# Performance work log

Measured on AMD Instinct MI355X. Metric: run time of the kernel, lower is better.

Reference implementation:

```python
import jax, jax.numpy as jnp
import numpy as np

DIM = 2048
N_HEADS = 16
HEAD_DIM = 128
KV_HEADS = 1
ROPE_BASE = 10000.0


def _rope_tables(T, dim, dtype):
    inv_freq = 1.0 / (ROPE_BASE ** (jnp.arange(0, dim, 2, dtype=jnp.float32) / dim))
    t = jnp.arange(T, dtype=jnp.float32)
    freqs = jnp.einsum('i,j->ij', t, inv_freq)          # [T, dim/2]
    emb = jnp.concatenate([freqs, freqs], axis=-1)      # [T, dim]
    cos = jnp.cos(emb)[None, None, :, :].astype(dtype)  # [1,1,T,dim]
    sin = jnp.sin(emb)[None, None, :, :].astype(dtype)
    return cos, sin


def _rotate_half(x):
    x1, x2 = jnp.split(x, 2, axis=-1)
    return jnp.concatenate([-x2, x1], axis=-1)


def setup_inputs() -> dict:
    key = jax.random.key(0)
    k1, k2, k3, k4, k5 = jax.random.split(key, 5)
    B, T = 2, 2048
    x = jax.random.normal(k1, (B, T, DIM), dtype=jnp.float32)
    # additive causal mask: 0 on/below diagonal, -1e9 above
    causal = jnp.triu(jnp.full((T, T), -1e9, dtype=jnp.float32), k=1)
    attn_mask = causal[None, None, :, :]
    s = 1.0 / np.sqrt(DIM)
    wq = jax.random.normal(k2, (DIM, N_HEADS * HEAD_DIM), dtype=jnp.float32) * s
    wk = jax.random.normal(k3, (DIM, KV_HEADS * HEAD_DIM), dtype=jnp.float32) * s
    wv = jax.random.normal(k4, (DIM, KV_HEADS * HEAD_DIM), dtype=jnp.float32) * s
    wo = jax.random.normal(k5, (N_HEADS * HEAD_DIM, DIM), dtype=jnp.float32) * s
    return {"x": x, "attn_mask": attn_mask, "wq": wq, "wk": wk, "wv": wv, "wo": wo}


def reference(x, attn_mask, wq, wk, wv, wo):
    B, T, C = x.shape
    q = (x @ wq).reshape(B, T, N_HEADS, HEAD_DIM).transpose(0, 2, 1, 3)   # [B,H,T,d]
    k = (x @ wk).reshape(B, T, KV_HEADS, HEAD_DIM).transpose(0, 2, 1, 3)  # [B,1,T,d]
    v = (x @ wv).reshape(B, T, KV_HEADS, HEAD_DIM).transpose(0, 2, 1, 3)  # [B,1,T,d]
    cos, sin = _rope_tables(T, HEAD_DIM, x.dtype)
    q = q * cos + _rotate_half(q) * sin
    k = k * cos + _rotate_half(k) * sin
    # KV head broadcasts over the H dim inside matmul (MQA expand path)
    att = jnp.matmul(q, k.swapaxes(-1, -2)) / np.sqrt(HEAD_DIM)          # [B,H,T,T]
    att = att + attn_mask
    w = jax.nn.softmax(att, axis=-1)
    y = jnp.matmul(w, v)                                                  # [B,H,T,d]
    y = y.transpose(0, 2, 1, 3).reshape(B, T, N_HEADS * HEAD_DIM)
    y = y @ wo
    k_exp = jnp.broadcast_to(k, (B, N_HEADS, T, HEAD_DIM))
    v_exp = jnp.broadcast_to(v, (B, N_HEADS, T, HEAD_DIM))
    return y, k_exp, v_exp
```

## Files before the change

kernel.cpp:

```cpp
#include <hip/hip_runtime.h>
#include <hip/hip_bf16.h>
#include <cstdint>
#include <cstddef>

#define B_SZ   2
#define T_SEQ  2048
#define C_DIM  2048
#define NH     16
#define HD     128

typedef __attribute__((ext_vector_type(8))) short s8v;
typedef __attribute__((ext_vector_type(4))) float f32x4;

typedef __attribute__((address_space(3))) char lds_char;
typedef __attribute__((address_space(1))) const char glob_char;

#define QSCALE 0.12751887f

__device__ __forceinline__ unsigned short f2bf(float f) {
    union { float f; uint32_t i; } v; v.f = f;
    uint32_t r = (v.i + 0x7FFFu + ((v.i >> 16) & 1u)) >> 16;
    return (unsigned short)r;
}

__device__ __forceinline__ unsigned int cvt2_bf16(float a, float b) {
    unsigned int w;
    asm("v_cvt_pk_bf16_f32 %0, %1, %2" : "=v"(w) : "v"(a), "v"(b));
    return w;
}

__global__ __launch_bounds__(256) void k_prep(
        const float* __restrict__ x, unsigned short* __restrict__ xb,
        float* __restrict__ cosT, float* __restrict__ sinT,
        float* __restrict__ cosT2, float* __restrict__ sinT2,
        const float* __restrict__ wq, const float* __restrict__ wk,
        const float* __restrict__ wv, const float* __restrict__ wo,
        unsigned short* __restrict__ wT, unsigned short* __restrict__ woT) {
    __shared__ unsigned short tile[64][66];
    int blk = blockIdx.x;
    int tid = threadIdx.x;

    if (blk < 2048) {
        int i = blk * 256 + tid;
        const int n4 = 4096 * 2048 / 4;
        const int stride = 2048 * 256;
        for (; i < n4; i += stride) {
            float4 v = reinterpret_cast<const float4*>(x)[i];
            ushort4 o;
            o.x = f2bf(v.x); o.y = f2bf(v.y); o.z = f2bf(v.z); o.w = f2bf(v.w);
            reinterpret_cast<ushort4*>(xb)[i] = o;
        }
        return;
    }
    blk -= 2048;
    if (blk < 512) {
        int idx = blk * 256 + tid;
        int t = idx >> 6, i = idx & 63;
        float inv = powf(10000.0f, -(float)i / 64.0f);
        float ang = (float)t * inv;
        float c = cosf(ang), s = sinf(ang);
        cosT[idx] = c;  sinT[idx] = s;
        cosT2[i * T_SEQ + t] = c;  sinT2[i * T_SEQ + t] = s;
        return;
    }
    blk -= 512;

    const float* in; unsigned short* out; int C, ldo, bx, by;
    if (blk < 1024) {
        in = wq; out = wT; C = 2048; ldo = 2048;
        bx = blk & 31; by = blk >> 5;
    } else if (blk < 1088) {
        int l = blk - 1024;
        in = wk; out = wT + (size_t)2048 * 2048; C = 128; ldo = 2048;
        bx = l & 1; by = l >> 1;
    } else if (blk < 1152) {
        int l = blk - 1088;
        in = wv; out = wT + (size_t)2176 * 2048; C = 128; ldo = 2048;
        bx = l & 1; by = l >> 1;
    } else {
        int l = blk - 1152;
        in = wo; out = woT; C = 2048; ldo = 2048;
        bx = l & 31; by = l >> 5;
    }
    int x0 = bx * 64, y0 = by * 64;
    int tx = tid & 63, ty = tid >> 6;
#pragma unroll
    for (int j = 0; j < 16; ++j) {
        int r = y0 + ty + j * 4;
        tile[ty + j * 4][tx] = f2bf(in[(size_t)r * C + x0 + tx]);
    }
    __syncthreads();
#pragma unroll
    for (int j = 0; j < 16; ++j) {
        int orow = x0 + ty + j * 4;
        out[(size_t)orow * ldo + y0 + tx] = tile[tx][ty + j * 4];
    }
}

#define BM 128
#define BN 128
#define BK 64

__global__ __launch_bounds__(256) void k_gemm_bt(
        const unsigned short* __restrict__ A,
        const unsigned short* __restrict__ Bt,
        float* __restrict__ C, int M, int N, int K, int ldc, int gx) {
    __shared__ char smem[BM * BK * 2 + BN * BK * 2];
    char* As = smem;
    char* Bs = smem + BM * BK * 2;
    int tid = threadIdx.x, lane = tid & 63, wid = tid >> 6;
    int nwg = gridDim.x, cpx = nwg >> 3;
    int orig = blockIdx.x;
    int wg = (orig & 7) * cpx + (orig >> 3);
    int bx = wg % gx, by = wg / gx;
    int m0 = by * BM, n0 = bx * BN;
    int wr = wid >> 1, wc = wid & 1;

    f32x4 acc[4][4] = {};

    int srow = wid * 32 + (lane >> 3);
    int cp = lane & 7;

    for (int k0 = 0; k0 < K; k0 += BK) {
#pragma unroll
        for (int i = 0; i < 4; ++i) {
            int row = srow + i * 8;
            int c = cp ^ (row & 7);
            const unsigned short* ga = A + (size_t)(m0 + row) * K + k0 + c * 8;
            const unsigned short* gb = Bt + (size_t)(n0 + row) * K + k0 + c * 8;
            __builtin_amdgcn_global_load_lds((glob_char*)ga,
                (lds_char*)(As + wid * 4096 + i * 1024), 16, 0, 0);
            __builtin_amdgcn_global_load_lds((glob_char*)gb,
                (lds_char*)(Bs + wid * 4096 + i * 1024), 16, 0, 0);
        }
        __syncthreads();

#pragma unroll
        for (int kc = 0; kc < 2; ++kc) {
            s8v af[4], bfr[4];
#pragma unroll
            for (int mi = 0; mi < 4; ++mi) {
                int row = wr * 64 + mi * 16 + (lane & 15);
                int slot = (kc * 4 + (lane >> 4)) ^ (row & 7);
                af[mi] = *reinterpret_cast<const s8v*>(As + row * 128 + slot * 16);
            }
#pragma unroll
            for (int ni = 0; ni < 4; ++ni) {
                int row = wc * 64 + ni * 16 + (lane & 15);
                int slot = (kc * 4 + (lane >> 4)) ^ (row & 7);
                bfr[ni] = *reinterpret_cast<const s8v*>(Bs + row * 128 + slot * 16);
            }
#pragma unroll
            for (int mi = 0; mi < 4; ++mi)
#pragma unroll
                for (int ni = 0; ni < 4; ++ni)
                    acc[mi][ni] = __builtin_amdgcn_mfma_f32_16x16x32_bf16(
                        af[mi], bfr[ni], acc[mi][ni], 0, 0, 0);
        }
        __syncthreads();
    }

#pragma unroll
    for (int mi = 0; mi < 4; ++mi) {
        int row = m0 + wr * 64 + mi * 16 + ((lane >> 4) << 2);
#pragma unroll
        for (int ni = 0; ni < 4; ++ni) {
            int col = n0 + wc * 64 + ni * 16 + (lane & 15);
            float* cp2 = C + (size_t)row * ldc + col;
#pragma unroll
            for (int r = 0; r < 4; ++r)
                cp2[(size_t)r * ldc] = acc[mi][ni][r];
        }
    }
}

__global__ __launch_bounds__(256) void k_gemm_qkv(
        const unsigned short* __restrict__ A,
        const unsigned short* __restrict__ Bt,
        const float* __restrict__ cosT2,
        const float* __restrict__ sinT2,
        unsigned short* __restrict__ qB,
        float* __restrict__ qkvKV) {
    const int GX = 18, K = 2048;
    __shared__ char smem[BM * BK * 2 + BN * BK * 2];
    char* As = smem;
    char* Bs = smem + BM * BK * 2;
    int tid = threadIdx.x, lane = tid & 63, wid = tid >> 6;
    int nwg = gridDim.x, cpx = nwg >> 3;
    int orig = blockIdx.x;
    int wg = (orig & 7) * cpx + (orig >> 3);
    int bx = wg % GX, by = wg / GX;
    int m0 = by * BM, n0 = bx * BN;
    int l15 = lane & 15, l4 = lane >> 4;

    f32x4 acc[2][8] = {};

    int srow = wid * 32 + (lane >> 3);
    int cp = lane & 7;

    for (int k0 = 0; k0 < K; k0 += BK) {
#pragma unroll
        for (int i = 0; i < 4; ++i) {
            int row = srow + i * 8;
            int c = cp ^ (row & 7);
            const unsigned short* ga = A + (size_t)(m0 + row) * K + k0 + c * 8;
            const unsigned short* gb = Bt + (size_t)(n0 + row) * K + k0 + c * 8;
            __builtin_amdgcn_global_load_lds((glob_char*)ga,
                (lds_char*)(As + wid * 4096 + i * 1024), 16, 0, 0);
            __builtin_amdgcn_global_load_lds((glob_char*)gb,
                (lds_char*)(Bs + wid * 4096 + i * 1024), 16, 0, 0);
        }
        __syncthreads();

#pragma unroll
        for (int kc = 0; kc < 2; ++kc) {
            s8v af[2], bfr[8];
#pragma unroll
            for (int mi = 0; mi < 2; ++mi) {
                int row = wid * 32 + mi * 16 + l15;
                int slot = (kc * 4 + l4) ^ (row & 7);
                af[mi] = *reinterpret_cast<const s8v*>(As + row * 128 + slot * 16);
            }
#pragma unroll
            for (int ni = 0; ni < 8; ++ni) {
                int row = ni * 16 + l15;
                int slot = (kc * 4 + l4) ^ (row & 7);
                bfr[ni] = *reinterpret_cast<const s8v*>(Bs + row * 128 + slot * 16);
            }
#pragma unroll
            for (int mi = 0; mi < 2; ++mi)
#pragma unroll
                for (int ni = 0; ni < 8; ++ni)
                    acc[mi][ni] = __builtin_amdgcn_mfma_f32_16x16x32_bf16(
                        af[mi], bfr[ni], acc[mi][ni], 0, 0, 0);
        }
        __syncthreads();
    }

    if (bx < 16) {
        int b = m0 >> 11, h = bx;
#pragma unroll
        for (int mi = 0; mi < 2; ++mi) {
            int t0 = (m0 + wid * 32 + mi * 16 + l4 * 4) & (T_SEQ - 1);
#pragma unroll
            for (int nip = 0; nip < 4; ++nip) {
                int d = nip * 16 + l15;
                float4 c4 = *reinterpret_cast<const float4*>(cosT2 + (size_t)d * T_SEQ + t0);
                float4 s4 = *reinterpret_cast<const float4*>(sinT2 + (size_t)d * T_SEQ + t0);
#pragma unroll
                for (int r = 0; r < 4; ++r) {
                    float x1 = acc[mi][nip][r];
                    float x2 = acc[mi][nip + 4][r];
                    float cc = (&c4.x)[r], ss = (&s4.x)[r];
                    float o1 = (x1 * cc - x2 * ss) * QSCALE;
                    float o2 = (x2 * cc + x1 * ss) * QSCALE;
                    size_t qoff = ((size_t)(b * NH + h) * T_SEQ + t0 + r) * HD + 2 * d;
                    *reinterpret_cast<unsigned int*>(qB + qoff) = cvt2_bf16(o1, o2);
                }
            }
        }
    } else {
        int colb = (bx - 16) * 128;
#pragma unroll
        for (int mi = 0; mi < 2; ++mi) {
            int row = m0 + wid * 32 + mi * 16 + l4 * 4;
#pragma unroll
            for (int ni = 0; ni < 8; ++ni) {
                int col = colb + ni * 16 + l15;
                float* cp2 = qkvKV + (size_t)row * 256 + col;
#pragma unroll
                for (int r = 0; r < 4; ++r)
                    cp2[(size_t)r * 256] = acc[mi][ni][r];
            }
        }
    }
}

__global__ __launch_bounds__(192) void k_kv_transform(
                               const float* __restrict__ qkvKV,
                               const float* __restrict__ cosT,
                               const float* __restrict__ sinT,
                               unsigned short* __restrict__ kB,
                               unsigned short* __restrict__ vT,
                               float* __restrict__ kexp,
                               float* __restrict__ vexp) {
    int bt = blockIdx.x;
    int b = bt >> 11, t = bt & 2047;
    int tid = threadIdx.x;
    const float* base = qkvKV + (size_t)bt * 256;

    if (tid < 64) {
        int d = tid;
        float c = cosT[t * 64 + d], s = sinT[t * 64 + d];
        float k1 = base[d], k2 = base[d + 64];
        float o1 = k1 * c - k2 * s;
        float o2 = k2 * c + k1 * s;
        size_t koff = ((size_t)b * T_SEQ + t) * HD + 2 * d;
        *reinterpret_cast<unsigned int*>(kB + koff) = cvt2_bf16(o1, o2);
#pragma unroll
        for (int h = 0; h < NH; ++h) {
            size_t eoff = ((size_t)(b * NH + h) * T_SEQ + t) * HD + d;
            kexp[eoff] = o1;
            kexp[eoff + 64] = o2;
        }
    } else {
        int d = tid - 64;
        float v = base[128 + d];
        vT[((size_t)b * HD + d) * T_SEQ + t] = f2bf(v);
#pragma unroll
        for (int h = 0; h < NH; ++h)
            vexp[((size_t)(b * NH + h) * T_SEQ + t) * HD + d] = v;
    }
}

__global__ __launch_bounds__(256, 3) void k_flash_attn(
        const unsigned short* __restrict__ qB,
        const unsigned short* __restrict__ kB,
        const unsigned short* __restrict__ vT,
        unsigned short* __restrict__ yattn) {
    __shared__ char smem[49152];
    int tid = threadIdx.x, lane = tid & 63, wvid = tid >> 6;
    int l15 = lane & 15, l4 = lane >> 4;
    int blk = blockIdx.x;
    int bh = blk & 31;
    int b = bh >> 4, h = bh & 15;
    int g = blk >> 5;
    int a = g & 7, qq = g >> 3;
    int u = (qq == 0) ? (31 - a) : (qq == 1) ? (16 + a)
          : (qq == 2) ? (15 - a) : a;
    int qrow0 = u * 64 + wvid * 16;

    const unsigned short* kbB   = kB + (size_t)b * T_SEQ * HD;
    const unsigned short* vbase = vT + (size_t)b * HD * T_SEQ;

    const unsigned short* qbase =
        qB + ((size_t)(b * NH + h) * T_SEQ + qrow0) * HD;
    s8v aq[4];
#pragma unroll
    for (int kc = 0; kc < 4; ++kc)
        aq[kc] = *reinterpret_cast<const s8v*>(
            qbase + (size_t)l15 * HD + kc * 32 + l4 * 8);

    float m = -3e38f, l = 0.f;
    f32x4 o[8] = {};

    int NT = 2 * u + 2;

    auto stage = [&](int buf, int t) {
        int kv0 = t * 32;
        char* kdst = smem + buf * 16384;
        char* vdst = smem + buf * 16384 + 8192;
#pragma unroll
        for (int j = 0; j < 2; ++j) {
            int n = j * 256 + tid;
            int row = n >> 4, ch = n & 15;
            const unsigned short* src =
                kbB + (size_t)(kv0 + row) * HD + (ch ^ (row & 7)) * 8;
            __builtin_amdgcn_global_load_lds((glob_char*)src,
                (lds_char*)(kdst + j * 4096 + wvid * 1024), 16, 0, 0);
        }
#pragma unroll
        for (int j = 0; j < 2; ++j) {
            int n = j * 256 + tid;
            int row = n >> 2, ch = n & 3;
            const unsigned short* src =
                vbase + (size_t)row * T_SEQ + kv0 + (ch ^ ((row >> 1) & 3)) * 8;
            __builtin_amdgcn_global_load_lds((glob_char*)src,
                (lds_char*)(vdst + j * 4096 + wvid * 1024), 16, 0, 0);
        }
    };

    stage(0, 0);
    stage(1, 1);
    asm volatile("s_waitcnt vmcnt(4)" ::: "memory");
    __builtin_amdgcn_s_barrier();
    __builtin_amdgcn_sched_barrier(0);

    int cur = 0;
    for (int t = 0; t < NT; ++t) {
        int nb = cur + 2; if (nb >= 3) nb -= 3;
        if (t + 2 < NT) stage(nb, t + 2);
        int kv0 = t * 32;
        const char* Kc = smem + cur * 16384;
        const char* Vc = smem + cur * 16384 + 8192;
        int act = (kv0 <= qrow0 + 15);

        if (act) {
            f32x4 sfr[2] = {};
            __builtin_amdgcn_s_setprio(1);
#pragma unroll
            for (int kc = 0; kc < 4; ++kc) {
                s8v kf[2];
#pragma unroll
                for (int n = 0; n < 2; ++n) {
                    int row = n * 16 + l15;
                    int byte = row * 256 +
                        ((kc * 64 + l4 * 16) ^ ((row & 7) << 4));
                    kf[n] = *reinterpret_cast<const s8v*>(Kc + byte);
                }
#pragma unroll
                for (int n = 0; n < 2; ++n)
                    sfr[n] = __builtin_amdgcn_mfma_f32_16x16x32_bf16(
                        kf[n], aq[kc], sfr[n], 0, 0, 0);
            }
            __builtin_amdgcn_s_setprio(0);

            if (kv0 + 31 > qrow0) {
                int qa = qrow0 + l15;
#pragma unroll
                for (int n = 0; n < 2; ++n)
#pragma unroll
                    for (int r = 0; r < 4; ++r) {
                        int kv = kv0 + n * 16 + l4 * 4 + r;
                        if (kv > qa) sfr[n][r] = -1e9f;
                    }
            }

            float pm = sfr[0][0];
#pragma unroll
            for (int r = 1; r < 4; ++r) pm = fmaxf(pm, sfr[0][r]);
#pragma unroll
            for (int r = 0; r < 4; ++r) pm = fmaxf(pm, sfr[1][r]);
            pm = fmaxf(pm, __shfl_xor(pm, 16));
            pm = fmaxf(pm, __shfl_xor(pm, 32));
            if (!__all(pm <= m + 8.0f)) {
                float mn = fmaxf(m, pm);
                float al = exp2f(m - mn);
                l *= al;
#pragma unroll
                for (int ds = 0; ds < 8; ++ds)
#pragma unroll
                    for (int r = 0; r < 4; ++r) o[ds][r] *= al;
                m = mn;
            }
#pragma unroll
            for (int n = 0; n < 2; ++n)
#pragma unroll
                for (int r = 0; r < 4; ++r) {
                    float p = exp2f(sfr[n][r] - m);
                    sfr[n][r] = p;
                    l += p;
                }

            unsigned int a0 = cvt2_bf16(sfr[0][0], sfr[0][1]);
            unsigned int a1 = cvt2_bf16(sfr[0][2], sfr[0][3]);
            unsigned int b0 = cvt2_bf16(sfr[1][0], sfr[1][1]);
            unsigned int b1 = cvt2_bf16(sfr[1][2], sfr[1][3]);
            int srcE = (lane & 15) | ((lane & 16) << 1);
            int srcO = srcE + 16;
            unsigned int ae0 = __shfl(a0, srcE), ae1 = __shfl(a1, srcE);
            unsigned int be0 = __shfl(b0, srcE), be1 = __shfl(b1, srcE);
            unsigned int ao0 = __shfl(a0, srcO), ao1 = __shfl(a1, srcO);
            unsigned int bo0 = __shfl(b0, srcO), bo1 = __shfl(b1, srcO);
            bool lo = (lane & 32) == 0;
            union { unsigned int u[4]; s8v v; } pf;
            pf.u[0] = lo ? ae0 : be0;
            pf.u[1] = lo ? ae1 : be1;
            pf.u[2] = lo ? ao0 : bo0;
            pf.u[3] = lo ? ao1 : bo1;

            __builtin_amdgcn_s_setprio(1);
#pragma unroll
            for (int ds = 0; ds < 8; ++ds) {
                int vrow = ds * 16 + l15;
                int vbyte = vrow * 64 + ((l4 * 16) ^ (((vrow >> 1) & 3) << 4));
                s8v bv = *reinterpret_cast<const s8v*>(Vc + vbyte);
                o[ds] = __builtin_amdgcn_mfma_f32_16x16x32_bf16(
                    bv, pf.v, o[ds], 0, 0, 0);
            }
            __builtin_amdgcn_s_setprio(0);
        }

        if (t + 2 < NT) {
            asm volatile("s_waitcnt vmcnt(4) lgkmcnt(0)" ::: "memory");
        } else {
            asm volatile("s_waitcnt vmcnt(0) lgkmcnt(0)" ::: "memory");
        }
        __builtin_amdgcn_s_barrier();
        __builtin_amdgcn_sched_barrier(0);
        cur = (cur == 2) ? 0 : cur + 1;
    }

    l += __shfl_xor(l, 16);
    l += __shfl_xor(l, 32);
    float inv = 1.0f / l;
    size_t rowoff = ((size_t)b * T_SEQ + qrow0 + l15) * C_DIM + h * HD;
#pragma unroll
    for (int ds = 0; ds < 8; ++ds) {
        uint2 w;
        w.x = cvt2_bf16(o[ds][0] * inv, o[ds][1] * inv);
        w.y = cvt2_bf16(o[ds][2] * inv, o[ds][3] * inv);
        *reinterpret_cast<uint2*>(yattn + rowoff + ds * 16 + l4 * 4) = w;
    }
}

extern "C" void kernel_launch(void* const* d_in, const int* in_sizes, int n_in,
                              void* d_out, int out_size, void* d_ws, size_t ws_size,
                              hipStream_t stream) {
    const float* x  = (const float*)d_in[0];
    const float* wq = (const float*)d_in[2];
    const float* wk = (const float*)d_in[3];
    const float* wv = (const float*)d_in[4];
    const float* wo = (const float*)d_in[5];

    char* ws = (char*)d_ws;
    size_t off = 0;
    auto alloc = [&](size_t bytes) -> void* {
        void* p = ws + off;
        off += (bytes + 255) & ~(size_t)255;
        return p;
    };
    unsigned short* xb    = (unsigned short*)alloc((size_t)4096 * 2048 * 2);
    unsigned short* wT    = (unsigned short*)alloc((size_t)2304 * 2048 * 2);
    unsigned short* woT   = (unsigned short*)alloc((size_t)2048 * 2048 * 2);
    float*          qkvKV = (float*)alloc((size_t)4096 * 256 * 4);
    float*          cosT  = (float*)alloc((size_t)2048 * 64 * 4);
    float*          sinT  = (float*)alloc((size_t)2048 * 64 * 4);
    float*          cosT2 = (float*)alloc((size_t)64 * 2048 * 4);
    float*          sinT2 = (float*)alloc((size_t)64 * 2048 * 4);
    unsigned short* qB    = (unsigned short*)alloc((size_t)2 * 16 * 2048 * 128 * 2);
    unsigned short* kB    = (unsigned short*)alloc((size_t)2 * 2048 * 128 * 2);
    unsigned short* vT    = (unsigned short*)alloc((size_t)2 * 128 * 2048 * 2);
    unsigned short* yattn = (unsigned short*)alloc((size_t)4096 * 2048 * 2);

    float* y_out = (float*)d_out;
    float* kexp  = y_out + (size_t)2 * 2048 * 2048;
    float* vexp  = kexp + (size_t)2 * 16 * 2048 * 128;

    k_prep<<<4736, 256, 0, stream>>>(x, xb, cosT, sinT, cosT2, sinT2,
                                     wq, wk, wv, wo, wT, woT);
    k_gemm_qkv<<<576, 256, 0, stream>>>(xb, wT, cosT2, sinT2, qB, qkvKV);
    k_kv_transform<<<4096, 192, 0, stream>>>(qkvKV, cosT, sinT, kB, vT, kexp, vexp);
    k_flash_attn<<<1024, 256, 0, stream>>>(qB, kB, vT, yattn);
    k_gemm_bt<<<512, 256, 0, stream>>>(
        yattn, woT, y_out, 4096, 2048, 2048, 2048, 16);
}
```

Measured before the change: 230.8 us.

## Use 2x2 wave tiling in QKV GEMM with LDS exchange for RoPE pairs

Changes the QKV projection GEMM's per-wave tile from 32x128 (4 waves stacked on M) to a 2x2 arrangement of 64x64 tiles. This cuts the LDS fragment reads per MFMA: each wave now loads 4 A and 4 B fragments instead of 2 and 8. Because RoPE pairs dimension d with d+64, the half-dimension partner now lives in another wave. The wc==1 waves therefore write their accumulators to an enlarged padded LDS buffer, and the wc==0 waves apply the rotation. This adds an extra barrier and LDS traffic in the epilogue, and leaves half the waves idle during the Q store.

```diff
diff --git a/kernel.cpp b/kernel.cpp
--- a/kernel.cpp
+++ b/kernel.cpp
@@ -182,7 +182,7 @@
         unsigned short* __restrict__ qB,
         float* __restrict__ qkvKV) {
     const int GX = 18, K = 2048;
-    __shared__ char smem[BM * BK * 2 + BN * BK * 2];
+    __shared__ char smem[34816];
     char* As = smem;
     char* Bs = smem + BM * BK * 2;
     int tid = threadIdx.x, lane = tid & 63, wid = tid >> 6;
@@ -192,8 +192,9 @@
     int bx = wg % GX, by = wg / GX;
     int m0 = by * BM, n0 = bx * BN;
     int l15 = lane & 15, l4 = lane >> 4;
-
-    f32x4 acc[2][8] = {};
+    int wr = wid >> 1, wc = wid & 1;
+
+    f32x4 acc[4][4] = {};
 
     int srow = wid * 32 + (lane >> 3);
     int cp = lane & 7;
@@ -214,23 +215,23 @@
 
 #pragma unroll
         for (int kc = 0; kc < 2; ++kc) {
-            s8v af[2], bfr[8];
-#pragma unroll
-            for (int mi = 0; mi < 2; ++mi) {
-                int row = wid * 32 + mi * 16 + l15;
+            s8v af[4], bfr[4];
+#pragma unroll
+            for (int mi = 0; mi < 4; ++mi) {
+                int row = wr * 64 + mi * 16 + l15;
                 int slot = (kc * 4 + l4) ^ (row & 7);
                 af[mi] = *reinterpret_cast<const s8v*>(As + row * 128 + slot * 16);
             }
 #pragma unroll
-            for (int ni = 0; ni < 8; ++ni) {
-                int row = ni * 16 + l15;
+            for (int ni = 0; ni < 4; ++ni) {
+                int row = wc * 64 + ni * 16 + l15;
                 int slot = (kc * 4 + l4) ^ (row & 7);
                 bfr[ni] = *reinterpret_cast<const s8v*>(Bs + row * 128 + slot * 16);
             }
 #pragma unroll
-            for (int mi = 0; mi < 2; ++mi)
-#pragma unroll
-                for (int ni = 0; ni < 8; ++ni)
+            for (int mi = 0; mi < 4; ++mi)
+#pragma unroll
+                for (int ni = 0; ni < 4; ++ni)
                     acc[mi][ni] = __builtin_amdgcn_mfma_f32_16x16x32_bf16(
                         af[mi], bfr[ni], acc[mi][ni], 0, 0, 0);
         }
@@ -238,35 +239,55 @@
     }
 
     if (bx < 16) {
-        int b = m0 >> 11, h = bx;
-#pragma unroll
-        for (int mi = 0; mi < 2; ++mi) {
-            int t0 = (m0 + wid * 32 + mi * 16 + l4 * 4) & (T_SEQ - 1);
-#pragma unroll
-            for (int nip = 0; nip < 4; ++nip) {
-                int d = nip * 16 + l15;
-                float4 c4 = *reinterpret_cast<const float4*>(cosT2 + (size_t)d * T_SEQ + t0);
-                float4 s4 = *reinterpret_cast<const float4*>(sinT2 + (size_t)d * T_SEQ + t0);
-#pragma unroll
-                for (int r = 0; r < 4; ++r) {
-                    float x1 = acc[mi][nip][r];
-                    float x2 = acc[mi][nip + 4][r];
-                    float cc = (&c4.x)[r], ss = (&s4.x)[r];
-                    float o1 = (x1 * cc - x2 * ss) * QSCALE;
-                    float o2 = (x2 * cc + x1 * ss) * QSCALE;
-                    size_t qoff = ((size_t)(b * NH + h) * T_SEQ + t0 + r) * HD + 2 * d;
-                    *reinterpret_cast<unsigned int*>(qB + qoff) = cvt2_bf16(o1, o2);
+        float* xch = reinterpret_cast<float*>(smem);
+        if (wc == 1) {
+            float* base = xch + ((size_t)wr * 64 + lane) * 68;
+#pragma unroll
+            for (int mi = 0; mi < 4; ++mi)
+#pragma unroll
+                for (int ni = 0; ni < 4; ++ni)
+                    *reinterpret_cast<f32x4*>(base + mi * 16 + ni * 4) =
+                        acc[mi][ni];
+        }
+        __syncthreads();
+        if (wc == 0) {
+            int b = m0 >> 11, h = bx;
+            const float* pbase = xch + ((size_t)wr * 64 + lane) * 68;
+#pragma unroll
+            for (int mi = 0; mi < 4; ++mi) {
+                int t0 = ((m0 & (T_SEQ - 1)) + wr * 64 + mi * 16 + l4 * 4);
+#pragma unroll
+                for (int ni = 0; ni < 4; ++ni) {
+                    int d = ni * 16 + l15;
+                    float4 c4 = *reinterpret_cast<const float4*>(
+                        cosT2 + (size_t)d * T_SEQ + t0);
+                    float4 s4 = *reinterpret_cast<const float4*>(
+                        sinT2 + (size_t)d * T_SEQ + t0);
+                    f32x4 px = *reinterpret_cast<const f32x4*>(
+                        pbase + mi * 16 + ni * 4);
+#pragma unroll
+                    for (int r = 0; r < 4; ++r) {
+                        float x1 = acc[mi][ni][r];
+                        float x2 = px[r];
+                        float cc = (&c4.x)[r], ss = (&s4.x)[r];
+                        float o1 = (x1 * cc - x2 * ss) * QSCALE;
+                        float o2 = (x2 * cc + x1 * ss) * QSCALE;
+                        size_t qoff = ((size_t)(b * NH + h) * T_SEQ + t0 + r)
+                                      * HD + 2 * d;
+                        *reinterpret_cast<unsigned int*>(qB + qoff) =
+                            cvt2_bf16(o1, o2);
+                    }
                 }
             }
         }
     } else {
         int colb = (bx - 16) * 128;
 #pragma unroll
-        for (int mi = 0; mi < 2; ++mi) {
-            int row = m0 + wid * 32 + mi * 16 + l4 * 4;
-#pragma unroll
-            for (int ni = 0; ni < 8; ++ni) {
-                int col = colb + ni * 16 + l15;
+        for (int mi = 0; mi < 4; ++mi) {
+            int row = m0 + wr * 64 + mi * 16 + l4 * 4;
+#pragma unroll
+            for (int ni = 0; ni < 4; ++ni) {
+                int col = colb + wc * 64 + ni * 16 + l15;
                 float* cp2 = qkvKV + (size_t)row * 256 + col;
 #pragma unroll
                 for (int r = 0; r < 4; ++r)
```

Result: no change. 229.4 us (median of 3 runs) (-0.6%).
